# Performance work log

Hardware: AMD Instinct MI355X
Metric: run time of the kernel (lower is better)

## Reference

```python
import jax, jax.numpy as jnp
import numpy as np

TAU = 0.05
MASK_VAL = -1000000000.0
EPS = 1e-12  # torch F.normalize eps


def _l2norm(x):
    n = jnp.linalg.norm(x, axis=-1, keepdims=True)
    return x / jnp.maximum(n, EPS)


def setup_inputs() -> dict:
    key = jax.random.key(0)
    k1, k2 = jax.random.split(key)
    N, D = 16384, 64
    z1 = jax.random.normal(k1, (N, D), dtype=jnp.float32)
    z2 = jax.random.normal(k2, (N, D), dtype=jnp.float32)
    return {"z1": z1, "z2": z2}


def reference(z1, z2):
    # normalize both views
    z1n = _l2norm(z1)
    z2n = _l2norm(z2)
    N = z1n.shape[0]
    # full similarity matrix [N, N]
    sim = jnp.einsum("nd,md->nm", z1n, z2n) / TAU
    pos = jnp.diagonal(sim)  # sim(z1[i], z2[i]) / tau
    # mask the positive position inside the negatives block (as the torch code does)
    eye = jnp.eye(N, dtype=bool)
    neg = jnp.where(eye, MASK_VAL, sim)
    # logits = [pos, masked row]; label = 0 -> CE = logsumexp(logits) - pos
    logits = jnp.concatenate([pos[:, None], neg], axis=1)  # [N, N+1]
    lse = jax.nn.logsumexp(logits, axis=1)
    loss = jnp.sum(lse - pos) / N
    return loss
```

## Files before the change

kernel.cpp:

```cpp
#include <hip/hip_runtime.h>
#include <hip/hip_bf16.h>


typedef __bf16  bf16x8 __attribute__((ext_vector_type(8)));
typedef __bf16  bf16x4 __attribute__((ext_vector_type(4)));
typedef float   f32x4  __attribute__((ext_vector_type(4)));

#if __has_builtin(__builtin_amdgcn_exp2f)
#define EXP2F(x) __builtin_amdgcn_exp2f(x)
#else
#define EXP2F(x) exp2f(x)
#endif
#if __has_builtin(__builtin_amdgcn_logf)
#define LOG2F(x) __builtin_amdgcn_logf(x)
#else
#define LOG2F(x) log2f(x)
#endif

#define DDIM   64
#define TILEB  2048
#define NSETS  4
#define NW     4
#define BM     (NW * NSETS * 16)
#define CS     32

__global__ __launch_bounds__(256) void norm_frag_kernel(
    const float* __restrict__ z1, const float* __restrict__ z2,
    __hip_bfloat16* __restrict__ z1f, __hip_bfloat16* __restrict__ z2f,
    float* __restrict__ rowsum, float* __restrict__ out,
    float scale1, int N)
{
    const int tid  = threadIdx.x;
    const int r    = tid >> 4, c = tid & 15;
    const int tile = blockIdx.x;
    const size_t row = (size_t)tile * 16 + r;
    const size_t off = (size_t)tile * TILEB
                     + ((c >> 3) << 10) + (((c >> 1) & 3) << 8)
                     + (r << 4) + ((c & 1) << 3);

    {
        float4 v = *(const float4*)(z1 + row * DDIM + c * 4);
        float ss = v.x*v.x + v.y*v.y + v.z*v.z + v.w*v.w;
        #pragma unroll
        for (int o = 8; o; o >>= 1) ss += __shfl_xor(ss, o);
        float inv = scale1 / fmaxf(sqrtf(ss), 1e-12f);
        bf16x4 ov = { __float2bfloat16(v.x*inv), __float2bfloat16(v.y*inv),
                      __float2bfloat16(v.z*inv), __float2bfloat16(v.w*inv) };
        *(bf16x4*)((char*)z1f + off) = ov;
    }
    {
        float4 v = *(const float4*)(z2 + row * DDIM + c * 4);
        float ss = v.x*v.x + v.y*v.y + v.z*v.z + v.w*v.w;
        #pragma unroll
        for (int o = 8; o; o >>= 1) ss += __shfl_xor(ss, o);
        float inv = 1.0f / fmaxf(sqrtf(ss), 1e-12f);
        bf16x4 ov = { __float2bfloat16(v.x*inv), __float2bfloat16(v.y*inv),
                      __float2bfloat16(v.z*inv), __float2bfloat16(v.w*inv) };
        *(bf16x4*)((char*)z2f + off) = ov;
    }

    if (tid < 16) rowsum[(size_t)tile * 16 + tid] = 0.f;
    if (tile == 0 && tid == 0) *out = 0.f;
}

__global__ __launch_bounds__(256) void infonce_main_kernel(
    const __hip_bfloat16* __restrict__ z1f,
    const __hip_bfloat16* __restrict__ z2f,
    float* __restrict__ rowsum,
    float* __restrict__ posv,
    int N)
{
    const int tid  = threadIdx.x;
    const int wave = tid >> 6;
    const int lane = tid & 63;
    const int q    = lane >> 4;
    const int l15  = lane & 15;

    const int colspan = N / CS;
    const int c0      = blockIdx.y * colspan;
    const int wr      = blockIdx.x * BM + wave * (NSETS * 16);

    bf16x8 a0[NSETS], a1[NSETS];
    #pragma unroll
    for (int s = 0; s < NSETS; ++s) {
        const char* ab = (const char*)z1f + (size_t)((wr >> 4) + s) * TILEB + lane * 16;
        a0[s] = *(const bf16x8*)(ab);
        a1[s] = *(const bf16x8*)(ab + 1024);
    }

    float sum[NSETS * 4];
    #pragma unroll
    for (int k = 0; k < NSETS * 4; ++k) sum[k] = 0.f;

    const char* bptr = (const char*)z2f + (size_t)(c0 >> 4) * TILEB + lane * 16;
    const int ntiles = colspan >> 4;

    #pragma unroll 2
    for (int t = 0; t < ntiles; ++t) {
        bf16x8 b0 = *(const bf16x8*)(bptr);
        bf16x8 b1 = *(const bf16x8*)(bptr + 1024);
        bptr += TILEB;
        const int cg = c0 + (t << 4);
        #pragma unroll
        for (int s = 0; s < NSETS; ++s) {
            f32x4 acc = {0.f, 0.f, 0.f, 0.f};
            acc = __builtin_amdgcn_mfma_f32_16x16x32_bf16(a0[s], b0, acc, 0, 0, 0);
            acc = __builtin_amdgcn_mfma_f32_16x16x32_bf16(a1[s], b1, acc, 0, 0, 0);
            if (cg == wr + s * 16) {
                #pragma unroll
                for (int i = 0; i < 4; ++i)
                    if (l15 == q * 4 + i) posv[cg + q * 4 + i] = acc[i];
            }
            sum[s * 4 + 0] += EXP2F(acc[0]);
            sum[s * 4 + 1] += EXP2F(acc[1]);
            sum[s * 4 + 2] += EXP2F(acc[2]);
            sum[s * 4 + 3] += EXP2F(acc[3]);
        }
    }

    #pragma unroll
    for (int k = 0; k < NSETS * 4; ++k) {
        float v = sum[k];
        #pragma unroll
        for (int o = 1; o < 16; o <<= 1) v += __shfl_xor(v, o);
        sum[k] = v;
    }
    if (l15 == 0) {
        #pragma unroll
        for (int s = 0; s < NSETS; ++s)
            #pragma unroll
            for (int i = 0; i < 4; ++i)
                atomicAdd(&rowsum[wr + s * 16 + q * 4 + i], sum[s * 4 + i]);
    }
}

__global__ __launch_bounds__(256) void finalize_kernel(
    const float* __restrict__ rowsum, const float* __restrict__ posv,
    float* __restrict__ out, int N)
{
    int row = blockIdx.x * 256 + threadIdx.x;
    float acc = (LOG2F(rowsum[row]) - posv[row]) * (0.69314718055994531f / (float)N);
    #pragma unroll
    for (int o = 32; o; o >>= 1) acc += __shfl_xor(acc, o);
    if ((threadIdx.x & 63) == 0) atomicAdd(out, acc);
}

extern "C" void kernel_launch(void* const* d_in, const int* in_sizes, int n_in,
                              void* d_out, int out_size, void* d_ws, size_t ws_size,
                              hipStream_t stream)
{
    const float* z1 = (const float*)d_in[0];
    const float* z2 = (const float*)d_in[1];
    const int N = in_sizes[0] / DDIM;

    char* ws = (char*)d_ws;
    __hip_bfloat16* z1f = (__hip_bfloat16*)ws;
    __hip_bfloat16* z2f = z1f + (size_t)N * DDIM;
    float* rowsum = (float*)(ws + 2 * (size_t)N * DDIM * 2);
    float* posv   = rowsum + N;

    const float kScale = 28.853900817779268f;

    norm_frag_kernel<<<N / 16, 256, 0, stream>>>(z1, z2, z1f, z2f, rowsum,
                                                 (float*)d_out, kScale, N);

    dim3 grid(N / BM, CS);
    infonce_main_kernel<<<grid, NW * 64, 0, stream>>>(z1f, z2f, rowsum, posv, N);

    finalize_kernel<<<N / 256, 256, 0, stream>>>(rowsum, posv, (float*)d_out, N);
}
```

Before: 115.4 us.

## Prefetch B fragments, move positive logits to norm kernel, fuse finalize via last-block

Computes the positive-pair dot product in the normalization kernel from the bf16 values, which removes the per-tile diagonal check from the main loop. The main loop now double-buffers two column tiles of B in registers and prefetches the next pair while issuing MFMAs, and adds an occupancy hint to launch bounds. The finalize kernel is replaced by a last-block-done counter inside the main kernel, saving one launch. The risks are higher register pressure from the prefetch and a serial tail, since one block reduces all N rows.

```diff
diff --git a/kernel.cpp b/kernel.cpp
--- a/kernel.cpp
+++ b/kernel.cpp
@@ -27,8 +27,8 @@
 __global__ __launch_bounds__(256) void norm_frag_kernel(
     const float* __restrict__ z1, const float* __restrict__ z2,
     __hip_bfloat16* __restrict__ z1f, __hip_bfloat16* __restrict__ z2f,
-    float* __restrict__ rowsum, float* __restrict__ out,
-    float scale1, int N)
+    float* __restrict__ rowsum, float* __restrict__ posv,
+    int* __restrict__ donecnt, float scale1, int N)
 {
     const int tid  = threadIdx.x;
     const int r    = tid >> 4, c = tid & 15;
@@ -38,15 +38,16 @@
                      + ((c >> 3) << 10) + (((c >> 1) & 3) << 8)
                      + (r << 4) + ((c & 1) << 3);
 
+    bf16x4 o1, o2;
     {
         float4 v = *(const float4*)(z1 + row * DDIM + c * 4);
         float ss = v.x*v.x + v.y*v.y + v.z*v.z + v.w*v.w;
         #pragma unroll
         for (int o = 8; o; o >>= 1) ss += __shfl_xor(ss, o);
         float inv = scale1 / fmaxf(sqrtf(ss), 1e-12f);
-        bf16x4 ov = { __float2bfloat16(v.x*inv), __float2bfloat16(v.y*inv),
-                      __float2bfloat16(v.z*inv), __float2bfloat16(v.w*inv) };
-        *(bf16x4*)((char*)z1f + off) = ov;
+        o1 = (bf16x4){ __float2bfloat16(v.x*inv), __float2bfloat16(v.y*inv),
+                       __float2bfloat16(v.z*inv), __float2bfloat16(v.w*inv) };
+        *(bf16x4*)((char*)z1f + off) = o1;
     }
     {
         float4 v = *(const float4*)(z2 + row * DDIM + c * 4);
@@ -54,21 +55,28 @@
         #pragma unroll
         for (int o = 8; o; o >>= 1) ss += __shfl_xor(ss, o);
         float inv = 1.0f / fmaxf(sqrtf(ss), 1e-12f);
-        bf16x4 ov = { __float2bfloat16(v.x*inv), __float2bfloat16(v.y*inv),
-                      __float2bfloat16(v.z*inv), __float2bfloat16(v.w*inv) };
-        *(bf16x4*)((char*)z2f + off) = ov;
-    }
+        o2 = (bf16x4){ __float2bfloat16(v.x*inv), __float2bfloat16(v.y*inv),
+                       __float2bfloat16(v.z*inv), __float2bfloat16(v.w*inv) };
+        *(bf16x4*)((char*)z2f + off) = o2;
+    }
+
+    float p = (float)o1[0]*(float)o2[0] + (float)o1[1]*(float)o2[1]
+            + (float)o1[2]*(float)o2[2] + (float)o1[3]*(float)o2[3];
+    #pragma unroll
+    for (int o = 8; o; o >>= 1) p += __shfl_xor(p, o);
+    if (c == 0) posv[row] = p;
 
     if (tid < 16) rowsum[(size_t)tile * 16 + tid] = 0.f;
-    if (tile == 0 && tid == 0) *out = 0.f;
+    if (tile == 0 && tid == 0) *donecnt = 0;
 }
 
-__global__ __launch_bounds__(256) void infonce_main_kernel(
+__global__ __launch_bounds__(256, 5) void infonce_main_kernel(
     const __hip_bfloat16* __restrict__ z1f,
     const __hip_bfloat16* __restrict__ z2f,
     float* __restrict__ rowsum,
-    float* __restrict__ posv,
-    int N)
+    const float* __restrict__ posv,
+    int* __restrict__ donecnt,
+    float* __restrict__ out, int N)
 {
     const int tid  = threadIdx.x;
     const int wave = tid >> 6;
@@ -77,6 +85,7 @@
     const int l15  = lane & 15;
 
     const int colspan = N / CS;
+    const int ntiles  = colspan >> 4;
     const int c0      = blockIdx.y * colspan;
     const int wr      = blockIdx.x * BM + wave * (NSETS * 16);
 
@@ -92,30 +101,41 @@
     #pragma unroll
     for (int k = 0; k < NSETS * 4; ++k) sum[k] = 0.f;
 
-    const char* bptr = (const char*)z2f + (size_t)(c0 >> 4) * TILEB + lane * 16;
-    const int ntiles = colspan >> 4;
-
-    #pragma unroll 2
-    for (int t = 0; t < ntiles; ++t) {
-        bf16x8 b0 = *(const bf16x8*)(bptr);
-        bf16x8 b1 = *(const bf16x8*)(bptr + 1024);
-        bptr += TILEB;
-        const int cg = c0 + (t << 4);
+    const char* bbase = (const char*)z2f + (size_t)(c0 >> 4) * TILEB + lane * 16;
+    const f32x4 kzero = {0.f, 0.f, 0.f, 0.f};
+
+    bf16x8 b0a = *(const bf16x8*)(bbase);
+    bf16x8 b1a = *(const bf16x8*)(bbase + 1024);
+    bf16x8 b0b = *(const bf16x8*)(bbase + TILEB);
+    bf16x8 b1b = *(const bf16x8*)(bbase + TILEB + 1024);
+
+    for (int t = 0; t < ntiles; t += 2) {
+        const char* pa = bbase + (size_t)((t + 2 < ntiles) ? t + 2 : 0) * TILEB;
+        const char* pb = bbase + (size_t)((t + 3 < ntiles) ? t + 3 : 0) * TILEB;
+        bf16x8 n0 = *(const bf16x8*)(pa);
+        bf16x8 n1 = *(const bf16x8*)(pa + 1024);
+        bf16x8 n2 = *(const bf16x8*)(pb);
+        bf16x8 n3 = *(const bf16x8*)(pb + 1024);
+
         #pragma unroll
         for (int s = 0; s < NSETS; ++s) {
-            f32x4 acc = {0.f, 0.f, 0.f, 0.f};
-            acc = __builtin_amdgcn_mfma_f32_16x16x32_bf16(a0[s], b0, acc, 0, 0, 0);
-            acc = __builtin_amdgcn_mfma_f32_16x16x32_bf16(a1[s], b1, acc, 0, 0, 0);
-            if (cg == wr + s * 16) {
-                #pragma unroll
-                for (int i = 0; i < 4; ++i)
-                    if (l15 == q * 4 + i) posv[cg + q * 4 + i] = acc[i];
-            }
+            f32x4 acc = __builtin_amdgcn_mfma_f32_16x16x32_bf16(a0[s], b0a, kzero, 0, 0, 0);
+            acc = __builtin_amdgcn_mfma_f32_16x16x32_bf16(a1[s], b1a, acc, 0, 0, 0);
             sum[s * 4 + 0] += EXP2F(acc[0]);
             sum[s * 4 + 1] += EXP2F(acc[1]);
             sum[s * 4 + 2] += EXP2F(acc[2]);
             sum[s * 4 + 3] += EXP2F(acc[3]);
         }
+        #pragma unroll
+        for (int s = 0; s < NSETS; ++s) {
+            f32x4 acc = __builtin_amdgcn_mfma_f32_16x16x32_bf16(a0[s], b0b, kzero, 0, 0, 0);
+            acc = __builtin_amdgcn_mfma_f32_16x16x32_bf16(a1[s], b1b, acc, 0, 0, 0);
+            sum[s * 4 + 0] += EXP2F(acc[0]);
+            sum[s * 4 + 1] += EXP2F(acc[1]);
+            sum[s * 4 + 2] += EXP2F(acc[2]);
+            sum[s * 4 + 3] += EXP2F(acc[3]);
+        }
+        b0a = n0; b1a = n1; b0b = n2; b1b = n3;
     }
 
     #pragma unroll
@@ -132,17 +152,31 @@
             for (int i = 0; i < 4; ++i)
                 atomicAdd(&rowsum[wr + s * 16 + q * 4 + i], sum[s * 4 + i]);
     }
-}
-
-__global__ __launch_bounds__(256) void finalize_kernel(
-    const float* __restrict__ rowsum, const float* __restrict__ posv,
-    float* __restrict__ out, int N)
-{
-    int row = blockIdx.x * 256 + threadIdx.x;
-    float acc = (LOG2F(rowsum[row]) - posv[row]) * (0.69314718055994531f / (float)N);
-    #pragma unroll
-    for (int o = 32; o; o >>= 1) acc += __shfl_xor(acc, o);
-    if ((threadIdx.x & 63) == 0) atomicAdd(out, acc);
+
+    __threadfence();
+    __shared__ int slast;
+    if (tid == 0) {
+        int done = atomicAdd(donecnt, 1);
+        slast = (done == (int)(gridDim.x * gridDim.y) - 1) ? 1 : 0;
+    }
+    __syncthreads();
+    if (slast) {
+        __threadfence();
+        float acc = 0.f;
+        for (int row = tid; row < N; row += 256) {
+            float s = __hip_atomic_load(&rowsum[row], __ATOMIC_RELAXED,
+                                        __HIP_MEMORY_SCOPE_AGENT);
+            acc += LOG2F(s) - posv[row];
+        }
+        #pragma unroll
+        for (int o = 32; o; o >>= 1) acc += __shfl_xor(acc, o);
+        __shared__ float red[NW];
+        if (lane == 0) red[wave] = acc;
+        __syncthreads();
+        if (tid == 0)
+            *out = 0.69314718055994531f * (red[0] + red[1] + red[2] + red[3])
+                 / (float)N;
+    }
 }
 
 extern "C" void kernel_launch(void* const* d_in, const int* in_sizes, int n_in,
@@ -156,16 +190,16 @@
     char* ws = (char*)d_ws;
     __hip_bfloat16* z1f = (__hip_bfloat16*)ws;
     __hip_bfloat16* z2f = z1f + (size_t)N * DDIM;
-    float* rowsum = (float*)(ws + 2 * (size_t)N * DDIM * 2);
-    float* posv   = rowsum + N;
+    float* rowsum  = (float*)(ws + 2 * (size_t)N * DDIM * 2);
+    float* posv    = rowsum + N;
+    int*   donecnt = (int*)(posv + N);
 
     const float kScale = 28.853900817779268f;
 
     norm_frag_kernel<<<N / 16, 256, 0, stream>>>(z1, z2, z1f, z2f, rowsum,
-                                                 (float*)d_out, kScale, N);
+                                                 posv, donecnt, kScale, N);
 
     dim3 grid(N / BM, CS);
-    infonce_main_kernel<<<grid, NW * 64, 0, stream>>>(z1f, z2f, rowsum, posv, N);
-
-    finalize_kernel<<<N / 256, 256, 0, stream>>>(rowsum, posv, (float*)d_out, N);
+    infonce_main_kernel<<<grid, NW * 64, 0, stream>>>(z1f, z2f, rowsum, posv,
+                                                      donecnt, (float*)d_out, N);
 }
```

Result: slower. 254.4 us (+120.5%).

## Compute positive logits in normalize kernel and drop diagonal check from MFMA loop

Applied to the files above, without the earlier changes.

The positive-pair dot products are now computed in the normalization kernel from the rounded bf16 values, using a 16-lane shuffle reduction. This removes the per-tile diagonal comparison and conditional store from the hot MFMA/exp loop. The main kernel also gains a launch-bounds occupancy hint of 8 and the inner loop unroll goes from 2 to 4. The output zeroing moves to a hipMemsetAsync, which adds one extra operation on the stream. The bf16 dot product should match the MFMA result up to accumulation order.

```diff
diff --git a/kernel.cpp b/kernel.cpp
--- a/kernel.cpp
+++ b/kernel.cpp
@@ -27,7 +27,7 @@
 __global__ __launch_bounds__(256) void norm_frag_kernel(
     const float* __restrict__ z1, const float* __restrict__ z2,
     __hip_bfloat16* __restrict__ z1f, __hip_bfloat16* __restrict__ z2f,
-    float* __restrict__ rowsum, float* __restrict__ out,
+    float* __restrict__ rowsum, float* __restrict__ posv,
     float scale1, int N)
 {
     const int tid  = threadIdx.x;
@@ -38,15 +38,16 @@
                      + ((c >> 3) << 10) + (((c >> 1) & 3) << 8)
                      + (r << 4) + ((c & 1) << 3);
 
+    bf16x4 o1, o2;
     {
         float4 v = *(const float4*)(z1 + row * DDIM + c * 4);
         float ss = v.x*v.x + v.y*v.y + v.z*v.z + v.w*v.w;
         #pragma unroll
         for (int o = 8; o; o >>= 1) ss += __shfl_xor(ss, o);
         float inv = scale1 / fmaxf(sqrtf(ss), 1e-12f);
-        bf16x4 ov = { __float2bfloat16(v.x*inv), __float2bfloat16(v.y*inv),
-                      __float2bfloat16(v.z*inv), __float2bfloat16(v.w*inv) };
-        *(bf16x4*)((char*)z1f + off) = ov;
+        o1 = (bf16x4){ __float2bfloat16(v.x*inv), __float2bfloat16(v.y*inv),
+                       __float2bfloat16(v.z*inv), __float2bfloat16(v.w*inv) };
+        *(bf16x4*)((char*)z1f + off) = o1;
     }
     {
         float4 v = *(const float4*)(z2 + row * DDIM + c * 4);
@@ -54,20 +55,24 @@
         #pragma unroll
         for (int o = 8; o; o >>= 1) ss += __shfl_xor(ss, o);
         float inv = 1.0f / fmaxf(sqrtf(ss), 1e-12f);
-        bf16x4 ov = { __float2bfloat16(v.x*inv), __float2bfloat16(v.y*inv),
-                      __float2bfloat16(v.z*inv), __float2bfloat16(v.w*inv) };
-        *(bf16x4*)((char*)z2f + off) = ov;
+        o2 = (bf16x4){ __float2bfloat16(v.x*inv), __float2bfloat16(v.y*inv),
+                       __float2bfloat16(v.z*inv), __float2bfloat16(v.w*inv) };
+        *(bf16x4*)((char*)z2f + off) = o2;
     }
 
+    float p = (float)o1[0]*(float)o2[0] + (float)o1[1]*(float)o2[1]
+            + (float)o1[2]*(float)o2[2] + (float)o1[3]*(float)o2[3];
+    #pragma unroll
+    for (int o = 8; o; o >>= 1) p += __shfl_xor(p, o);
+    if (c == 0) posv[row] = p;
+
     if (tid < 16) rowsum[(size_t)tile * 16 + tid] = 0.f;
-    if (tile == 0 && tid == 0) *out = 0.f;
 }
 
-__global__ __launch_bounds__(256) void infonce_main_kernel(
+__global__ __launch_bounds__(256, 8) void infonce_main_kernel(
     const __hip_bfloat16* __restrict__ z1f,
     const __hip_bfloat16* __restrict__ z2f,
     float* __restrict__ rowsum,
-    float* __restrict__ posv,
     int N)
 {
     const int tid  = threadIdx.x;
@@ -77,6 +82,7 @@
     const int l15  = lane & 15;
 
     const int colspan = N / CS;
+    const int ntiles  = colspan >> 4;
     const int c0      = blockIdx.y * colspan;
     const int wr      = blockIdx.x * BM + wave * (NSETS * 16);
 
@@ -93,24 +99,17 @@
     for (int k = 0; k < NSETS * 4; ++k) sum[k] = 0.f;
 
     const char* bptr = (const char*)z2f + (size_t)(c0 >> 4) * TILEB + lane * 16;
-    const int ntiles = colspan >> 4;
+    const f32x4 kzero = {0.f, 0.f, 0.f, 0.f};
 
-    #pragma unroll 2
+    #pragma unroll 4
     for (int t = 0; t < ntiles; ++t) {
         bf16x8 b0 = *(const bf16x8*)(bptr);
         bf16x8 b1 = *(const bf16x8*)(bptr + 1024);
         bptr += TILEB;
-        const int cg = c0 + (t << 4);
         #pragma unroll
         for (int s = 0; s < NSETS; ++s) {
-            f32x4 acc = {0.f, 0.f, 0.f, 0.f};
-            acc = __builtin_amdgcn_mfma_f32_16x16x32_bf16(a0[s], b0, acc, 0, 0, 0);
+            f32x4 acc = __builtin_amdgcn_mfma_f32_16x16x32_bf16(a0[s], b0, kzero, 0, 0, 0);
             acc = __builtin_amdgcn_mfma_f32_16x16x32_bf16(a1[s], b1, acc, 0, 0, 0);
-            if (cg == wr + s * 16) {
-                #pragma unroll
-                for (int i = 0; i < 4; ++i)
-                    if (l15 == q * 4 + i) posv[cg + q * 4 + i] = acc[i];
-            }
             sum[s * 4 + 0] += EXP2F(acc[0]);
             sum[s * 4 + 1] += EXP2F(acc[1]);
             sum[s * 4 + 2] += EXP2F(acc[2]);
@@ -161,11 +160,13 @@
 
     const float kScale = 28.853900817779268f;
 
+    hipMemsetAsync(d_out, 0, sizeof(float), stream);
+
     norm_frag_kernel<<<N / 16, 256, 0, stream>>>(z1, z2, z1f, z2f, rowsum,
-                                                 (float*)d_out, kScale, N);
+                                                 posv, kScale, N);
 
     dim3 grid(N / BM, CS);
-    infonce_main_kernel<<<grid, NW * 64, 0, stream>>>(z1f, z2f, rowsum, posv, N);
+    infonce_main_kernel<<<grid, NW * 64, 0, stream>>>(z1f, z2f, rowsum, N);
 
     finalize_kernel<<<N / 256, 256, 0, stream>>>(rowsum, posv, (float*)d_out, N);
 }
```

After: 111.0 us. 3.8% less time.
